# Kernel tuning notes

Hardware: AMD Instinct MI355X
Metric: run time of the kernel (lower is better)

## Reference

```python
import jax, jax.numpy as jnp
import numpy as np

N = 100000      # num nodes
R = 32          # num relations
E = 3200000     # num edges
F_IN = 128      # feat_len
H = 16          # hidden dim (hard-coded in source)
C = 8           # num classes


def setup_inputs() -> dict:
    key = jax.random.key(0)
    k1, k2, k3, k4, k5 = jax.random.split(key, 5)
    emb = jax.random.normal(k1, (N, F_IN), dtype=jnp.float32)
    W1 = jax.random.normal(k2, (R, F_IN, H), dtype=jnp.float32) * 0.05
    W2 = jax.random.normal(k3, (R, H, C), dtype=jnp.float32) * 0.05
    edge_index = jax.random.randint(k4, (2, E), 0, N, dtype=jnp.int64)
    edge_type = jax.random.randint(k5, (E,), 0, R, dtype=jnp.int64)
    return {"emb": emb, "W1": W1, "W2": W2,
            "edge_index": edge_index, "edge_type": edge_type}


def _rgcn_layer(x, W, src, dst, etype, edge_norm):
    # x: [N, Fin], W: [R, Fin, Fout]
    # Transform once per relation, then gather per edge (avoids [E,Fin,Fout]).
    xw = jnp.einsum('nf,rfo->rno', x, W)          # [R, N, Fout]
    msg = xw[etype, src] * edge_norm[:, None]      # [E, Fout]
    return jax.ops.segment_sum(msg, dst, num_segments=N)  # [N, Fout]


def reference(emb, W1, W2, edge_index, edge_type):
    src, dst = edge_index[0], edge_index[1]
    # PyG RGCNConv aggr='mean': normalize by per-(dst, relation) in-degree.
    key_idx = dst * R + edge_type                              # [E]
    deg = jax.ops.segment_sum(jnp.ones((E,), emb.dtype), key_idx,
                              num_segments=N * R)              # [N*R]
    edge_norm = 1.0 / jnp.maximum(deg, 1.0)
    edge_norm = edge_norm[key_idx]                             # [E]

    h = jax.nn.relu(_rgcn_layer(emb, W1, src, dst, edge_type, edge_norm))
    h = _rgcn_layer(h, W2, src, dst, edge_type, edge_norm)
    return jax.nn.log_softmax(h, axis=1)
```

## Files before the change

kernel.cpp:

```cpp
#include <hip/hip_runtime.h>
#include <hip/hip_bf16.h>
#include <math.h>

#define N_NODES 100000
#define R 32
#define E_EDGES 3200000
#define F_IN 128
#define HDIM 16
#define CDIM 8
#define NOUT 512
#define M_PAD 100032
#define NBUCK 391
#define CAP 9216
#define KEYS 8192
#define P1CHUNK 8192
#define CVT_BLKS 6252
#define PREP_BLKS 128
#define FRONT_GRID (NBUCK + CVT_BLKS + PREP_BLKS)
#define GEMM_BLKS 6252
#define MID_GRID (NBUCK + GEMM_BLKS)

typedef __attribute__((ext_vector_type(8))) short bf16x8;
typedef __attribute__((ext_vector_type(4))) float f32x4;
typedef __attribute__((ext_vector_type(2))) _Float16 f16x2;
typedef __attribute__((ext_vector_type(4))) _Float16 f16x4;

static __device__ __forceinline__ unsigned short f2bf(float f) {
    unsigned int u = __float_as_uint(f);
    unsigned int r = (u + 0x7FFFu + ((u >> 16) & 1u)) >> 16;
    return (unsigned short)r;
}
static __device__ __forceinline__ float bfl(unsigned x) {
    return __uint_as_float(x << 16);
}
static __device__ __forceinline__ float bfh(unsigned x) {
    return __uint_as_float(x & 0xFFFF0000u);
}
static __device__ __forceinline__ f16x2 asf16x2(float f) {
    union { float f; f16x2 h; } u; u.f = f; return u.h;
}

#if __has_builtin(__builtin_amdgcn_fdot2)
static __device__ __forceinline__ float FDOT2(f16x2 a, f16x2 b, float c) {
    return __builtin_amdgcn_fdot2(a, b, c, false);
}
#else
static __device__ __forceinline__ float FDOT2(f16x2 a, f16x2 b, float c) {
    return c + (float)a.x * (float)b.x + (float)a.y * (float)b.y;
}
#endif

__global__ __launch_bounds__(512) void k_front(const int* __restrict__ src,
                                               const int* __restrict__ dst,
                                               const int* __restrict__ et,
                                               const float* __restrict__ emb,
                                               const float* __restrict__ W1,
                                               int* __restrict__ gcursor,
                                               unsigned int* __restrict__ ebuf,
                                               unsigned short* __restrict__ ebf,
                                               unsigned short* __restrict__ BmT) {
    __shared__ int sh[3 * NBUCK];
    int b = blockIdx.x, t = threadIdx.x;
    if (b < NBUCK) {
        int* hist = sh;
        int* rank = sh + NBUCK;
        int* base = sh + 2 * NBUCK;
        for (int j = t; j < NBUCK; j += 512) { hist[j] = 0; rank[j] = 0; }
        __syncthreads();
        int e0 = b * P1CHUNK;
        int e1 = e0 + P1CHUNK; if (e1 > E_EDGES) e1 = E_EDGES;
        int n4 = (e1 - e0) >> 2;
        const int4* d4 = (const int4*)(dst + e0);
        const int4* s4 = (const int4*)(src + e0);
        const int4* t4 = (const int4*)(et + e0);
        for (int i = t; i < n4; i += 512) {
            int4 v = d4[i];
            atomicAdd(&hist[v.x >> 8], 1);
            atomicAdd(&hist[v.y >> 8], 1);
            atomicAdd(&hist[v.z >> 8], 1);
            atomicAdd(&hist[v.w >> 8], 1);
        }
        __syncthreads();
        for (int j = t; j < NBUCK; j += 512)
            base[j] = hist[j] ? atomicAdd(&gcursor[j], hist[j]) : 0;
        __syncthreads();
        for (int i = t; i < n4; i += 512) {
            int4 dv = d4[i];
            int4 sv = s4[i];
            int4 tv = t4[i];
            int ds[4] = {dv.x, dv.y, dv.z, dv.w};
            int ss[4] = {sv.x, sv.y, sv.z, sv.w};
            int ts[4] = {tv.x, tv.y, tv.z, tv.w};
            #pragma unroll
            for (int u = 0; u < 4; ++u) {
                int d = ds[u];
                int bk = d >> 8;
                unsigned pk = ((unsigned)(d & 255) << 22) | ((unsigned)ts[u] << 17)
                            | (unsigned)ss[u];
                int lr = atomicAdd(&rank[bk], 1);
                ebuf[(size_t)bk * CAP + base[bk] + lr] = pk;
            }
        }
    } else if (b < NBUCK + CVT_BLKS) {
        size_t base = ((size_t)(b - NBUCK) * 512 + t) * 4;
        int row = (int)(base >> 7);
        ushort4 o;
        if (row < N_NODES) {
            float4 a = *(const float4*)(emb + base);
            o.x = f2bf(a.x); o.y = f2bf(a.y); o.z = f2bf(a.z); o.w = f2bf(a.w);
        } else {
            o.x = o.y = o.z = o.w = 0;
        }
        *(ushort4*)(ebf + base) = o;
    } else {
        int i = (b - NBUCK - CVT_BLKS) * 512 + t;
        int n = i >> 7;
        int f = i & 127;
        int r = n >> 4;
        int o = n & 15;
        BmT[i] = f2bf(W1[r * (F_IN * HDIM) + f * HDIM + o]);
    }
}

__global__ __launch_bounds__(512) void k_scanb(const int* __restrict__ gcursor,
                                               int* __restrict__ bucketstart,
                                               int* __restrict__ rowstart) {
    __shared__ int sb[NBUCK + 1];
    int t = threadIdx.x;
    if (t == 0) {
        int acc = 0;
        for (int b = 0; b < NBUCK; ++b) { int v = gcursor[b]; sb[b] = acc; acc += v; }
        sb[NBUCK] = acc;
        rowstart[N_NODES] = acc;
    }
    __syncthreads();
    for (int j = t; j <= NBUCK; j += 512) bucketstart[j] = sb[j];
}

__global__ __launch_bounds__(256) void k_mid(const unsigned int* __restrict__ ebuf,
                                             const int* __restrict__ gcursor,
                                             const int* __restrict__ bucketstart,
                                             int* __restrict__ rowstart,
                                             unsigned int* __restrict__ elist,
                                             const unsigned short* __restrict__ Abf,
                                             const unsigned short* __restrict__ BmT,
                                             unsigned short* __restrict__ C) {
    __shared__ __align__(16) char smem[52224 + 64];
    int b = blockIdx.x, t = threadIdx.x;
    if (b < NBUCK) {
        unsigned int* cnt = (unsigned int*)smem;
        int* wsum = (int*)(smem + 32768);
        int cntE = gcursor[b];
        size_t esrc = (size_t)b * CAP;
        int e0 = bucketstart[b];
        #pragma unroll
        for (int j = 0; j < KEYS / 256; ++j) cnt[t + j * 256] = 0;
        __syncthreads();
        for (int i = t; i < cntE; i += 256)
            atomicAdd(&cnt[ebuf[esrc + i] >> 17], 1u);
        __syncthreads();
        int kbase = t * (KEYS / 256);
        int s = 0;
        #pragma unroll
        for (int j = 0; j < KEYS / 256; ++j) s += (int)cnt[kbase + j];
        int lane = t & 63, wv = t >> 6;
        int sc = s;
        #pragma unroll
        for (int off = 1; off < 64; off <<= 1) {
            int v = __shfl_up(sc, off, 64);
            if (lane >= off) sc += v;
        }
        if (lane == 63) wsum[wv] = sc;
        __syncthreads();
        if (t == 0) {
            int a = 0;
            #pragma unroll
            for (int w = 0; w < 4; ++w) { int v = wsum[w]; wsum[w] = a; a += v; }
        }
        __syncthreads();
        int run = wsum[wv] + sc - s;
        #pragma unroll
        for (int j = 0; j < KEYS / 256; ++j) {
            unsigned v = cnt[kbase + j];
            unsigned lc = v > 1023u ? 1023u : v;
            cnt[kbase + j] = (unsigned)run | (lc << 20);
            run += (int)v;
        }
        __syncthreads();
        {
            int d = b * 256 + t;
            if (d < N_NODES) rowstart[d] = e0 + (int)(cnt[t * 32] & 0xFFFFFu);
        }
        __syncthreads();
        for (int i = t; i < cntE; i += 256) {
            unsigned pk = ebuf[esrc + i];
            int key = pk >> 17;
            unsigned vv = atomicAdd(&cnt[key], 1u);
            int pos = (int)(vv & 0xFFFFFu);
            unsigned len = (vv >> 20) & 1023u;
            elist[e0 + pos] = (pk & 0x3FFFFFu) | (len << 22);
        }
    } else {
        unsigned short* As = (unsigned short*)smem;
        unsigned short* Bs = (unsigned short*)(smem + 17408);
        int bb = b - NBUCK;
        int row0 = (bb >> 2) * 64;
        int col0 = (bb & 3) * 128;
        #pragma unroll
        for (int j = 0; j < 4; ++j) {
            int idx = t + j * 256;
            int r = idx >> 4;
            int u = idx & 15;
            float4 v = *(const float4*)(Abf + (size_t)(row0 + r) * F_IN + u * 8);
            *(float4*)(&As[r * 136 + u * 8]) = v;
        }
        #pragma unroll
        for (int j = 0; j < 8; ++j) {
            int idx = t + j * 256;
            int r = idx >> 4;
            int u = idx & 15;
            float4 v = *(const float4*)(BmT + (size_t)(col0 + r) * F_IN + u * 8);
            *(float4*)(&Bs[r * 136 + u * 8]) = v;
        }
        __syncthreads();
        int w = t >> 6;
        int lane = t & 63;
        int q = lane >> 4;
        int mr = lane & 15;
        f32x4 acc[8] = {};
        const unsigned short* ap = &As[(w * 16 + mr) * 136 + q * 8];
        #pragma unroll
        for (int kk = 0; kk < 4; ++kk) {
            bf16x8 af = *(const bf16x8*)(ap + kk * 32);
            #pragma unroll
            for (int tt = 0; tt < 8; ++tt) {
                bf16x8 bf = *(const bf16x8*)(&Bs[(tt * 16 + mr) * 136 + q * 8 + kk * 32]);
                acc[tt] = __builtin_amdgcn_mfma_f32_16x16x32_bf16(af, bf, acc[tt], 0, 0, 0);
            }
        }
        #pragma unroll
        for (int tt = 0; tt < 8; ++tt) {
            #pragma unroll
            for (int j = 0; j < 4; ++j) {
                int row = row0 + w * 16 + q * 4 + j;
                C[(size_t)row * NOUT + col0 + tt * 16 + mr] = f2bf(acc[tt][j]);
            }
        }
    }
}

__global__ __launch_bounds__(256) void k_gather1(const int* __restrict__ rowstart,
                                                 const unsigned int* __restrict__ elist,
                                                 const unsigned short* __restrict__ xw1,
                                                 _Float16* __restrict__ h) {
    __shared__ float nlut[1024];
    int t = threadIdx.x;
    for (int j = t; j < 1024; j += 256) nlut[j] = 1.0f / (float)(j ? j : 1);
    __syncthreads();
    int g = t >> 2;
    int c = t & 3;
    int d = blockIdx.x * 64 + g;
    if (d >= N_NODES) return;
    int i = rowstart[d], end = rowstart[d + 1];
    float a0 = 0.f, a1 = 0.f, a2 = 0.f, a3 = 0.f;
    for (; i + 3 < end; i += 4) {
        unsigned pk0 = elist[i];
        unsigned pk1 = elist[i + 1];
        unsigned pk2 = elist[i + 2];
        unsigned pk3 = elist[i + 3];
        uint2 x0 = *(const uint2*)(xw1 + (size_t)(pk0 & 0x1FFFF) * NOUT + ((pk0 >> 17) & 31) * HDIM + c * 4);
        uint2 x1 = *(const uint2*)(xw1 + (size_t)(pk1 & 0x1FFFF) * NOUT + ((pk1 >> 17) & 31) * HDIM + c * 4);
        uint2 x2 = *(const uint2*)(xw1 + (size_t)(pk2 & 0x1FFFF) * NOUT + ((pk2 >> 17) & 31) * HDIM + c * 4);
        uint2 x3 = *(const uint2*)(xw1 + (size_t)(pk3 & 0x1FFFF) * NOUT + ((pk3 >> 17) & 31) * HDIM + c * 4);
        float n0 = nlut[pk0 >> 22], n1 = nlut[pk1 >> 22];
        float n2 = nlut[pk2 >> 22], n3 = nlut[pk3 >> 22];
        a0 += bfl(x0.x) * n0; a1 += bfh(x0.x) * n0; a2 += bfl(x0.y) * n0; a3 += bfh(x0.y) * n0;
        a0 += bfl(x1.x) * n1; a1 += bfh(x1.x) * n1; a2 += bfl(x1.y) * n1; a3 += bfh(x1.y) * n1;
        a0 += bfl(x2.x) * n2; a1 += bfh(x2.x) * n2; a2 += bfl(x2.y) * n2; a3 += bfh(x2.y) * n2;
        a0 += bfl(x3.x) * n3; a1 += bfh(x3.x) * n3; a2 += bfl(x3.y) * n3; a3 += bfh(x3.y) * n3;
    }
    for (; i < end; ++i) {
        unsigned pk = elist[i];
        uint2 x = *(const uint2*)(xw1 + (size_t)(pk & 0x1FFFF) * NOUT + ((pk >> 17) & 31) * HDIM + c * 4);
        float nm = nlut[pk >> 22];
        a0 += bfl(x.x) * nm; a1 += bfh(x.x) * nm; a2 += bfl(x.y) * nm; a3 += bfh(x.y) * nm;
    }
    f16x4 o;
    o.x = (_Float16)fmaxf(a0, 0.f);
    o.y = (_Float16)fmaxf(a1, 0.f);
    o.z = (_Float16)fmaxf(a2, 0.f);
    o.w = (_Float16)fmaxf(a3, 0.f);
    *(f16x4*)(h + (size_t)d * HDIM + c * 4) = o;
}

#define W2P 260
__global__ __launch_bounds__(256) void k_gather2(const int* __restrict__ rowstart,
                                                 const unsigned int* __restrict__ elist,
                                                 const _Float16* __restrict__ h,
                                                 const float* __restrict__ W2,
                                                 float* __restrict__ out) {
    __shared__ f16x2 sW2h[CDIM * W2P];
    __shared__ float nlut[1024];
    int t = threadIdx.x;
    for (int j = t; j < 1024; j += 256) nlut[j] = 1.0f / (float)(j ? j : 1);
    #pragma unroll
    for (int j = 0; j < 8; ++j) {
        int idx = t + j * 256;
        int c = idx >> 8;
        int rem = idx & 255;
        int r = rem >> 3;
        int jj = rem & 7;
        f16x2 p;
        p.x = (_Float16)W2[r * (HDIM * CDIM) + (2 * jj) * CDIM + c];
        p.y = (_Float16)W2[r * (HDIM * CDIM) + (2 * jj + 1) * CDIM + c];
        sW2h[c * W2P + rem] = p;
    }
    __syncthreads();

    int g = t >> 3;
    int c = t & 7;
    int d = blockIdx.x * 32 + g;
    if (d >= N_NODES) return;
    const f16x2* wc = &sW2h[c * W2P];
    int i = rowstart[d], end = rowstart[d + 1];
    float acc0 = 0.f, acc1 = 0.f;
    for (; i + 1 < end; i += 2) {
        unsigned pk0 = elist[i];
        unsigned pk1 = elist[i + 1];
        const float4* hp0 = (const float4*)(h + (size_t)(pk0 & 0x1FFFF) * HDIM);
        const float4* hp1 = (const float4*)(h + (size_t)(pk1 & 0x1FFFF) * HDIM);
        float4 u0 = hp0[0], u1 = hp0[1];
        float4 v0 = hp1[0], v1 = hp1[1];
        float nm0 = nlut[pk0 >> 22], nm1 = nlut[pk1 >> 22];
        const f16x2* wp0 = wc + ((pk0 >> 17) & 31) * 8;
        const f16x2* wp1 = wc + ((pk1 >> 17) & 31) * 8;
        float sd0 = 0.f, sd1 = 0.f;
        sd0 = FDOT2(asf16x2(u0.x), wp0[0], sd0);
        sd0 = FDOT2(asf16x2(u0.y), wp0[1], sd0);
        sd0 = FDOT2(asf16x2(u0.z), wp0[2], sd0);
        sd0 = FDOT2(asf16x2(u0.w), wp0[3], sd0);
        sd0 = FDOT2(asf16x2(u1.x), wp0[4], sd0);
        sd0 = FDOT2(asf16x2(u1.y), wp0[5], sd0);
        sd0 = FDOT2(asf16x2(u1.z), wp0[6], sd0);
        sd0 = FDOT2(asf16x2(u1.w), wp0[7], sd0);
        sd1 = FDOT2(asf16x2(v0.x), wp1[0], sd1);
        sd1 = FDOT2(asf16x2(v0.y), wp1[1], sd1);
        sd1 = FDOT2(asf16x2(v0.z), wp1[2], sd1);
        sd1 = FDOT2(asf16x2(v0.w), wp1[3], sd1);
        sd1 = FDOT2(asf16x2(v1.x), wp1[4], sd1);
        sd1 = FDOT2(asf16x2(v1.y), wp1[5], sd1);
        sd1 = FDOT2(asf16x2(v1.z), wp1[6], sd1);
        sd1 = FDOT2(asf16x2(v1.w), wp1[7], sd1);
        acc0 += nm0 * sd0;
        acc1 += nm1 * sd1;
    }
    if (i < end) {
        unsigned pk = elist[i];
        const float4* hp = (const float4*)(h + (size_t)(pk & 0x1FFFF) * HDIM);
        float4 u0 = hp[0], u1 = hp[1];
        float nm = nlut[pk >> 22];
        const f16x2* wp = wc + ((pk >> 17) & 31) * 8;
        float sd = 0.f;
        sd = FDOT2(asf16x2(u0.x), wp[0], sd);
        sd = FDOT2(asf16x2(u0.y), wp[1], sd);
        sd = FDOT2(asf16x2(u0.z), wp[2], sd);
        sd = FDOT2(asf16x2(u0.w), wp[3], sd);
        sd = FDOT2(asf16x2(u1.x), wp[4], sd);
        sd = FDOT2(asf16x2(u1.y), wp[5], sd);
        sd = FDOT2(asf16x2(u1.z), wp[6], sd);
        sd = FDOT2(asf16x2(u1.w), wp[7], sd);
        acc0 += nm * sd;
    }
    float acc = acc0 + acc1;
    float m = acc;
    #pragma unroll
    for (int mask = 1; mask < 8; mask <<= 1)
        m = fmaxf(m, __shfl_xor(m, mask, 8));
    float ex = expf(acc - m);
    float ssumv = ex;
    #pragma unroll
    for (int mask = 1; mask < 8; mask <<= 1)
        ssumv += __shfl_xor(ssumv, mask, 8);
    out[(size_t)d * CDIM + c] = acc - m - logf(ssumv);
}

extern "C" void kernel_launch(void* const* d_in, const int* in_sizes, int n_in,
                              void* d_out, int out_size, void* d_ws, size_t ws_size,
                              hipStream_t stream) {
    const float* emb = (const float*)d_in[0];
    const float* W1  = (const float*)d_in[1];
    const float* W2  = (const float*)d_in[2];
    const int* ei    = (const int*)d_in[3];
    const int* et    = (const int*)d_in[4];
    const int* srcp  = ei;
    const int* dstp  = ei + E_EDGES;

    char* ws = (char*)d_ws;
    size_t off = 0;
    #define ALIGN256(x) (((x) + 255) & ~(size_t)255)
    int* gcursor     = (int*)(ws + off); off = ALIGN256(off + 512 * 4);
    int* bucketstart = (int*)(ws + off); off = ALIGN256(off + 512 * 4);
    int* rowstart    = (int*)(ws + off); off = ALIGN256(off + ((size_t)N_NODES + 8) * 4);
    unsigned int* ebuf  = (unsigned int*)(ws + off); off = ALIGN256(off + (size_t)NBUCK * CAP * 4);
    unsigned int* elist = (unsigned int*)(ws + off); off = ALIGN256(off + (size_t)E_EDGES * 4);
    unsigned short* BmT  = (unsigned short*)(ws + off); off = ALIGN256(off + (size_t)NOUT * F_IN * 2);
    unsigned short* ebf  = (unsigned short*)(ws + off); off = ALIGN256(off + (size_t)M_PAD * F_IN * 2);
    unsigned short* xw1  = (unsigned short*)(ws + off); off = ALIGN256(off + (size_t)M_PAD * NOUT * 2);
    _Float16* h          = (_Float16*)(ws + off);       off = ALIGN256(off + (size_t)N_NODES * HDIM * 2);
    float* out = (float*)d_out;

    hipMemsetAsync(gcursor, 0, 512 * 4, stream);

    k_front<<<FRONT_GRID, 512, 0, stream>>>(srcp, dstp, et, emb, W1, gcursor, ebuf, ebf, BmT);
    k_scanb<<<1, 512, 0, stream>>>(gcursor, bucketstart, rowstart);
    k_mid<<<MID_GRID, 256, 0, stream>>>(ebuf, gcursor, bucketstart, rowstart, elist, ebf, BmT, xw1);
    k_gather1<<<(N_NODES + 63) / 64, 256, 0, stream>>>(rowstart, elist, xw1, h);
    k_gather2<<<(N_NODES + 31) / 32, 256, 0, stream>>>(rowstart, elist, h, W2, out);
}
```

Measured before the change: 332.6 us.

## Loop GEMM blocks over all columns; widen gather1 threads; unroll gather2 by four

The GEMM portion of k_mid now has each block load its 64-row A tile once and loop over the four 128-column B tiles, so there are a quarter as many blocks and less redundant A loading. gather1 now uses 8 threads per destination node, each reading 4 bytes instead of 8, and keeps separate accumulators per unrolled edge. This gives more threads per node and more independent load chains. gather2 unrolls its edge loop by four with independent accumulators to raise memory-level parallelism. The costs are extra syncthreads inside the GEMM loop, smaller per-thread loads in gather1, and higher register pressure in gather2.

```diff
diff --git a/kernel.cpp b/kernel.cpp
--- a/kernel.cpp
+++ b/kernel.cpp
@@ -17,13 +17,12 @@
 #define CVT_BLKS 6252
 #define PREP_BLKS 128
 #define FRONT_GRID (NBUCK + CVT_BLKS + PREP_BLKS)
-#define GEMM_BLKS 6252
+#define GEMM_BLKS 1563
 #define MID_GRID (NBUCK + GEMM_BLKS)
 
 typedef __attribute__((ext_vector_type(8))) short bf16x8;
 typedef __attribute__((ext_vector_type(4))) float f32x4;
 typedef __attribute__((ext_vector_type(2))) _Float16 f16x2;
-typedef __attribute__((ext_vector_type(4))) _Float16 f16x4;
 
 static __device__ __forceinline__ unsigned short f2bf(float f) {
     unsigned int u = __float_as_uint(f);
@@ -203,9 +202,7 @@
     } else {
         unsigned short* As = (unsigned short*)smem;
         unsigned short* Bs = (unsigned short*)(smem + 17408);
-        int bb = b - NBUCK;
-        int row0 = (bb >> 2) * 64;
-        int col0 = (bb & 3) * 128;
+        int row0 = (b - NBUCK) * 64;
         #pragma unroll
         for (int j = 0; j < 4; ++j) {
             int idx = t + j * 256;
@@ -214,36 +211,39 @@
             float4 v = *(const float4*)(Abf + (size_t)(row0 + r) * F_IN + u * 8);
             *(float4*)(&As[r * 136 + u * 8]) = v;
         }
-        #pragma unroll
-        for (int j = 0; j < 8; ++j) {
-            int idx = t + j * 256;
-            int r = idx >> 4;
-            int u = idx & 15;
-            float4 v = *(const float4*)(BmT + (size_t)(col0 + r) * F_IN + u * 8);
-            *(float4*)(&Bs[r * 136 + u * 8]) = v;
-        }
-        __syncthreads();
         int w = t >> 6;
         int lane = t & 63;
         int q = lane >> 4;
         int mr = lane & 15;
-        f32x4 acc[8] = {};
         const unsigned short* ap = &As[(w * 16 + mr) * 136 + q * 8];
-        #pragma unroll
-        for (int kk = 0; kk < 4; ++kk) {
-            bf16x8 af = *(const bf16x8*)(ap + kk * 32);
+        for (int col0 = 0; col0 < NOUT; col0 += 128) {
+            __syncthreads();
+            #pragma unroll
+            for (int j = 0; j < 8; ++j) {
+                int idx = t + j * 256;
+                int r = idx >> 4;
+                int u = idx & 15;
+                float4 v = *(const float4*)(BmT + (size_t)(col0 + r) * F_IN + u * 8);
+                *(float4*)(&Bs[r * 136 + u * 8]) = v;
+            }
+            __syncthreads();
+            f32x4 acc[8] = {};
+            #pragma unroll
+            for (int kk = 0; kk < 4; ++kk) {
+                bf16x8 af = *(const bf16x8*)(ap + kk * 32);
+                #pragma unroll
+                for (int tt = 0; tt < 8; ++tt) {
+                    bf16x8 bf = *(const bf16x8*)(&Bs[(tt * 16 + mr) * 136 + q * 8 + kk * 32]);
+                    acc[tt] = __builtin_amdgcn_mfma_f32_16x16x32_bf16(af, bf, acc[tt], 0, 0, 0);
+                }
+            }
             #pragma unroll
             for (int tt = 0; tt < 8; ++tt) {
-                bf16x8 bf = *(const bf16x8*)(&Bs[(tt * 16 + mr) * 136 + q * 8 + kk * 32]);
-                acc[tt] = __builtin_amdgcn_mfma_f32_16x16x32_bf16(af, bf, acc[tt], 0, 0, 0);
-            }
-        }
-        #pragma unroll
-        for (int tt = 0; tt < 8; ++tt) {
-            #pragma unroll
-            for (int j = 0; j < 4; ++j) {
-                int row = row0 + w * 16 + q * 4 + j;
-                C[(size_t)row * NOUT + col0 + tt * 16 + mr] = f2bf(acc[tt][j]);
+                #pragma unroll
+                for (int j = 0; j < 4; ++j) {
+                    int row = row0 + w * 16 + q * 4 + j;
+                    C[(size_t)row * NOUT + col0 + tt * 16 + mr] = f2bf(acc[tt][j]);
+                }
             }
         }
     }
@@ -257,40 +257,39 @@
     int t = threadIdx.x;
     for (int j = t; j < 1024; j += 256) nlut[j] = 1.0f / (float)(j ? j : 1);
     __syncthreads();
-    int g = t >> 2;
-    int c = t & 3;
-    int d = blockIdx.x * 64 + g;
+    int g = t >> 3;
+    int c = t & 7;
+    int d = blockIdx.x * 32 + g;
     if (d >= N_NODES) return;
     int i = rowstart[d], end = rowstart[d + 1];
-    float a0 = 0.f, a1 = 0.f, a2 = 0.f, a3 = 0.f;
+    float a0 = 0.f, a1 = 0.f, b0 = 0.f, b1 = 0.f;
+    float c0 = 0.f, c1 = 0.f, e0 = 0.f, e1 = 0.f;
     for (; i + 3 < end; i += 4) {
         unsigned pk0 = elist[i];
         unsigned pk1 = elist[i + 1];
         unsigned pk2 = elist[i + 2];
         unsigned pk3 = elist[i + 3];
-        uint2 x0 = *(const uint2*)(xw1 + (size_t)(pk0 & 0x1FFFF) * NOUT + ((pk0 >> 17) & 31) * HDIM + c * 4);
-        uint2 x1 = *(const uint2*)(xw1 + (size_t)(pk1 & 0x1FFFF) * NOUT + ((pk1 >> 17) & 31) * HDIM + c * 4);
-        uint2 x2 = *(const uint2*)(xw1 + (size_t)(pk2 & 0x1FFFF) * NOUT + ((pk2 >> 17) & 31) * HDIM + c * 4);
-        uint2 x3 = *(const uint2*)(xw1 + (size_t)(pk3 & 0x1FFFF) * NOUT + ((pk3 >> 17) & 31) * HDIM + c * 4);
+        unsigned x0 = *(const unsigned*)(xw1 + (size_t)(pk0 & 0x1FFFF) * NOUT + ((pk0 >> 17) & 31) * HDIM + c * 2);
+        unsigned x1 = *(const unsigned*)(xw1 + (size_t)(pk1 & 0x1FFFF) * NOUT + ((pk1 >> 17) & 31) * HDIM + c * 2);
+        unsigned x2 = *(const unsigned*)(xw1 + (size_t)(pk2 & 0x1FFFF) * NOUT + ((pk2 >> 17) & 31) * HDIM + c * 2);
+        unsigned x3 = *(const unsigned*)(xw1 + (size_t)(pk3 & 0x1FFFF) * NOUT + ((pk3 >> 17) & 31) * HDIM + c * 2);
         float n0 = nlut[pk0 >> 22], n1 = nlut[pk1 >> 22];
         float n2 = nlut[pk2 >> 22], n3 = nlut[pk3 >> 22];
-        a0 += bfl(x0.x) * n0; a1 += bfh(x0.x) * n0; a2 += bfl(x0.y) * n0; a3 += bfh(x0.y) * n0;
-        a0 += bfl(x1.x) * n1; a1 += bfh(x1.x) * n1; a2 += bfl(x1.y) * n1; a3 += bfh(x1.y) * n1;
-        a0 += bfl(x2.x) * n2; a1 += bfh(x2.x) * n2; a2 += bfl(x2.y) * n2; a3 += bfh(x2.y) * n2;
-        a0 += bfl(x3.x) * n3; a1 += bfh(x3.x) * n3; a2 += bfl(x3.y) * n3; a3 += bfh(x3.y) * n3;
+        a0 += bfl(x0) * n0; a1 += bfh(x0) * n0;
+        b0 += bfl(x1) * n1; b1 += bfh(x1) * n1;
+        c0 += bfl(x2) * n2; c1 += bfh(x2) * n2;
+        e0 += bfl(x3) * n3; e1 += bfh(x3) * n3;
     }
     for (; i < end; ++i) {
         unsigned pk = elist[i];
-        uint2 x = *(const uint2*)(xw1 + (size_t)(pk & 0x1FFFF) * NOUT + ((pk >> 17) & 31) * HDIM + c * 4);
+        unsigned x = *(const unsigned*)(xw1 + (size_t)(pk & 0x1FFFF) * NOUT + ((pk >> 17) & 31) * HDIM + c * 2);
         float nm = nlut[pk >> 22];
-        a0 += bfl(x.x) * nm; a1 += bfh(x.x) * nm; a2 += bfl(x.y) * nm; a3 += bfh(x.y) * nm;
-    }
-    f16x4 o;
-    o.x = (_Float16)fmaxf(a0, 0.f);
-    o.y = (_Float16)fmaxf(a1, 0.f);
-    o.z = (_Float16)fmaxf(a2, 0.f);
-    o.w = (_Float16)fmaxf(a3, 0.f);
-    *(f16x4*)(h + (size_t)d * HDIM + c * 4) = o;
+        a0 += bfl(x) * nm; a1 += bfh(x) * nm;
+    }
+    f16x2 o;
+    o.x = (_Float16)fmaxf(a0 + b0 + c0 + e0, 0.f);
+    o.y = (_Float16)fmaxf(a1 + b1 + c1 + e1, 0.f);
+    *(f16x2*)(h + (size_t)d * HDIM + c * 2) = o;
 }
 
 #define W2P 260
@@ -323,38 +322,65 @@
     if (d >= N_NODES) return;
     const f16x2* wc = &sW2h[c * W2P];
     int i = rowstart[d], end = rowstart[d + 1];
-    float acc0 = 0.f, acc1 = 0.f;
-    for (; i + 1 < end; i += 2) {
+    float acc0 = 0.f, acc1 = 0.f, acc2 = 0.f, acc3 = 0.f;
+    for (; i + 3 < end; i += 4) {
         unsigned pk0 = elist[i];
         unsigned pk1 = elist[i + 1];
+        unsigned pk2 = elist[i + 2];
+        unsigned pk3 = elist[i + 3];
         const float4* hp0 = (const float4*)(h + (size_t)(pk0 & 0x1FFFF) * HDIM);
         const float4* hp1 = (const float4*)(h + (size_t)(pk1 & 0x1FFFF) * HDIM);
+        const float4* hp2 = (const float4*)(h + (size_t)(pk2 & 0x1FFFF) * HDIM);
+        const float4* hp3 = (const float4*)(h + (size_t)(pk3 & 0x1FFFF) * HDIM);
         float4 u0 = hp0[0], u1 = hp0[1];
         float4 v0 = hp1[0], v1 = hp1[1];
+        float4 w0 = hp2[0], w1 = hp2[1];
+        float4 x0 = hp3[0], x1 = hp3[1];
         float nm0 = nlut[pk0 >> 22], nm1 = nlut[pk1 >> 22];
+        float nm2 = nlut[pk2 >> 22], nm3 = nlut[pk3 >> 22];
         const f16x2* wp0 = wc + ((pk0 >> 17) & 31) * 8;
         const f16x2* wp1 = wc + ((pk1 >> 17) & 31) * 8;
-        float sd0 = 0.f, sd1 = 0.f;
-        sd0 = FDOT2(asf16x2(u0.x), wp0[0], sd0);
-        sd0 = FDOT2(asf16x2(u0.y), wp0[1], sd0);
-        sd0 = FDOT2(asf16x2(u0.z), wp0[2], sd0);
-        sd0 = FDOT2(asf16x2(u0.w), wp0[3], sd0);
-        sd0 = FDOT2(asf16x2(u1.x), wp0[4], sd0);
-        sd0 = FDOT2(asf16x2(u1.y), wp0[5], sd0);
-        sd0 = FDOT2(asf16x2(u1.z), wp0[6], sd0);
-        sd0 = FDOT2(asf16x2(u1.w), wp0[7], sd0);
-        sd1 = FDOT2(asf16x2(v0.x), wp1[0], sd1);
-        sd1 = FDOT2(asf16x2(v0.y), wp1[1], sd1);
-        sd1 = FDOT2(asf16x2(v0.z), wp1[2], sd1);
-        sd1 = FDOT2(asf16x2(v0.w), wp1[3], sd1);
-        sd1 = FDOT2(asf16x2(v1.x), wp1[4], sd1);
-        sd1 = FDOT2(asf16x2(v1.y), wp1[5], sd1);
-        sd1 = FDOT2(asf16x2(v1.z), wp1[6], sd1);
-        sd1 = FDOT2(asf16x2(v1.w), wp1[7], sd1);
-        acc0 += nm0 * sd0;
-        acc1 += nm1 * sd1;
-    }
-    if (i < end) {
+        const f16x2* wp2 = wc + ((pk2 >> 17) & 31) * 8;
+        const f16x2* wp3 = wc + ((pk3 >> 17) & 31) * 8;
+        float s0 = 0.f, s1 = 0.f, s2 = 0.f, s3 = 0.f;
+        s0 = FDOT2(asf16x2(u0.x), wp0[0], s0);
+        s0 = FDOT2(asf16x2(u0.y), wp0[1], s0);
+        s0 = FDOT2(asf16x2(u0.z), wp0[2], s0);
+        s0 = FDOT2(asf16x2(u0.w), wp0[3], s0);
+        s0 = FDOT2(asf16x2(u1.x), wp0[4], s0);
+        s0 = FDOT2(asf16x2(u1.y), wp0[5], s0);
+        s0 = FDOT2(asf16x2(u1.z), wp0[6], s0);
+        s0 = FDOT2(asf16x2(u1.w), wp0[7], s0);
+        s1 = FDOT2(asf16x2(v0.x), wp1[0], s1);
+        s1 = FDOT2(asf16x2(v0.y), wp1[1], s1);
+        s1 = FDOT2(asf16x2(v0.z), wp1[2], s1);
+        s1 = FDOT2(asf16x2(v0.w), wp1[3], s1);
+        s1 = FDOT2(asf16x2(v1.x), wp1[4], s1);
+        s1 = FDOT2(asf16x2(v1.y), wp1[5], s1);
+        s1 = FDOT2(asf16x2(v1.z), wp1[6], s1);
+        s1 = FDOT2(asf16x2(v1.w), wp1[7], s1);
+        s2 = FDOT2(asf16x2(w0.x), wp2[0], s2);
+        s2 = FDOT2(asf16x2(w0.y), wp2[1], s2);
+        s2 = FDOT2(asf16x2(w0.z), wp2[2], s2);
+        s2 = FDOT2(asf16x2(w0.w), wp2[3], s2);
+        s2 = FDOT2(asf16x2(w1.x), wp2[4], s2);
+        s2 = FDOT2(asf16x2(w1.y), wp2[5], s2);
+        s2 = FDOT2(asf16x2(w1.z), wp2[6], s2);
+        s2 = FDOT2(asf16x2(w1.w), wp2[7], s2);
+        s3 = FDOT2(asf16x2(x0.x), wp3[0], s3);
+        s3 = FDOT2(asf16x2(x0.y), wp3[1], s3);
+        s3 = FDOT2(asf16x2(x0.z), wp3[2], s3);
+        s3 = FDOT2(asf16x2(x0.w), wp3[3], s3);
+        s3 = FDOT2(asf16x2(x1.x), wp3[4], s3);
+        s3 = FDOT2(asf16x2(x1.y), wp3[5], s3);
+        s3 = FDOT2(asf16x2(x1.z), wp3[6], s3);
+        s3 = FDOT2(asf16x2(x1.w), wp3[7], s3);
+        acc0 += nm0 * s0;
+        acc1 += nm1 * s1;
+        acc2 += nm2 * s2;
+        acc3 += nm3 * s3;
+    }
+    for (; i < end; ++i) {
         unsigned pk = elist[i];
         const float4* hp = (const float4*)(h + (size_t)(pk & 0x1FFFF) * HDIM);
         float4 u0 = hp[0], u1 = hp[1];
@@ -371,7 +397,7 @@
         sd = FDOT2(asf16x2(u1.w), wp[7], sd);
         acc0 += nm * sd;
     }
-    float acc = acc0 + acc1;
+    float acc = (acc0 + acc1) + (acc2 + acc3);
     float m = acc;
     #pragma unroll
     for (int mask = 1; mask < 8; mask <<= 1)
@@ -414,6 +440,6 @@
     k_front<<<FRONT_GRID, 512, 0, stream>>>(srcp, dstp, et, emb, W1, gcursor, ebuf, ebf, BmT);
     k_scanb<<<1, 512, 0, stream>>>(gcursor, bucketstart, rowstart);
     k_mid<<<MID_GRID, 256, 0, stream>>>(ebuf, gcursor, bucketstart, rowstart, elist, ebf, BmT, xw1);
-    k_gather1<<<(N_NODES + 63) / 64, 256, 0, stream>>>(rowstart, elist, xw1, h);
+    k_gather1<<<(N_NODES + 31) / 32, 256, 0, stream>>>(rowstart, elist, xw1, h);
     k_gather2<<<(N_NODES + 31) / 32, 256, 0, stream>>>(rowstart, elist, h, W2, out);
 }
```

Result: no change. 328.3 us (-1.3%).
